# Optimization experiments

Hardware: AMD Instinct MI355X
Metric: run time of the kernel (lower is better)

## Reference

```python
import jax, jax.numpy as jnp
import numpy as np
from jax import lax

H = W = 1024            # input frame size
STRIDE = 16             # backbone total stride (4 stride-2 convs)
FH = FW = H // STRIDE   # 64x64 feature map
A = 3                   # anchors per cell
SIZES = (32.0, 64.0, 128.0)
K = 100                 # fixed NMS candidate count (jit-static)
SCORE_TH = 0.5          # kwargs['threshhold']
IOU_TH = 0.5
BORDER = 4              # draw_boxes border_size=4


def _conv(x, w, b, stride):
    y = lax.conv_general_dilated(x, w, (stride, stride), 'SAME',
                                 dimension_numbers=('NCHW', 'OIHW', 'NCHW'))
    return y + b[None, :, None, None]


def _anchors():
    ys, xs = jnp.meshgrid(jnp.arange(FH, dtype=jnp.float32),
                          jnp.arange(FW, dtype=jnp.float32), indexing='ij')
    cx = (xs + 0.5) * STRIDE
    cy = (ys + 0.5) * STRIDE
    sz = jnp.asarray(SIZES, dtype=jnp.float32)
    cx = jnp.broadcast_to(cx[:, :, None], (FH, FW, A))
    cy = jnp.broadcast_to(cy[:, :, None], (FH, FW, A))
    ww = jnp.broadcast_to(sz[None, None, :], (FH, FW, A))
    return jnp.stack([cx, cy, ww, ww], -1).reshape(-1, 4)  # [N,4] cx,cy,w,h


def _facenet(frame, w1, b1, w2, b2, w3, b3, w4, b4, wh, bh):
    x = jax.nn.relu(_conv(frame, w1, b1, 2))   # [1,32,512,512]
    x = jax.nn.relu(_conv(x, w2, b2, 2))       # [1,64,256,256]
    x = jax.nn.relu(_conv(x, w3, b3, 2))       # [1,128,128,128]
    x = jax.nn.relu(_conv(x, w4, b4, 2))       # [1,256,64,64]
    p = _conv(x, wh, bh, 1)                    # [1,A*5,64,64]
    p = p.reshape(A, 5, FH, FW).transpose(2, 3, 0, 1).reshape(-1, 5)  # [N,5]
    t, logit = p[:, :4], p[:, 4]
    a = _anchors()
    cx = a[:, 0] + t[:, 0] * a[:, 2]
    cy = a[:, 1] + t[:, 1] * a[:, 3]
    bw = a[:, 2] * jnp.exp(jnp.clip(t[:, 2], -4.0, 4.0))
    bhh = a[:, 3] * jnp.exp(jnp.clip(t[:, 3], -4.0, 4.0))
    boxes = jnp.stack([cx - bw * 0.5, cy - bhh * 0.5,
                       cx + bw * 0.5, cy + bhh * 0.5], -1)  # [N,4] xyxy
    scores = jax.nn.sigmoid(logit)             # [N]
    return boxes, scores


def _pairwise_iou(b):
    area = (b[:, 2] - b[:, 0]) * (b[:, 3] - b[:, 1])
    lt = jnp.maximum(b[:, None, :2], b[None, :, :2])
    rb = jnp.minimum(b[:, None, 2:], b[None, :, 2:])
    wh2 = jnp.clip(rb - lt, 0.0)
    inter = wh2[..., 0] * wh2[..., 1]
    return inter / (area[:, None] + area[None, :] - inter + 1e-9)


def _nms(boxes, scores):
    s = jnp.where(scores >= SCORE_TH, scores, -1.0)
    top, idx = lax.top_k(s, K)
    b = boxes[idx]                    # [K,4], score-sorted
    valid = top > 0.0
    ious = _pairwise_iou(b)           # [K,K]
    rng = jnp.arange(K)

    def body(i, keep):
        sup = (ious[i] > IOU_TH) & keep[i] & (rng > i)
        return keep & (~sup)

    keep = lax.fori_loop(0, K, body, valid)
    return b, keep


def _draw(frame, boxes, keep):
    x1 = jnp.clip(boxes[:, 0], 0.0, W)[:, None, None]
    y1 = jnp.clip(boxes[:, 1], 0.0, H)[:, None, None]
    x2 = jnp.clip(boxes[:, 2], 0.0, W)[:, None, None]
    y2 = jnp.clip(boxes[:, 3], 0.0, H)[:, None, None]
    ys = jnp.arange(H, dtype=jnp.float32)[None, :, None]
    xs = jnp.arange(W, dtype=jnp.float32)[None, None, :]
    inside = (ys >= y1) & (ys < y2) & (xs >= x1) & (xs < x2)
    inner = (ys >= y1 + BORDER) & (ys < y2 - BORDER) & \
            (xs >= x1 + BORDER) & (xs < x2 - BORDER)
    border = inside & (~inner) & keep[:, None, None]   # [K,H,W]
    mask = jnp.any(border, axis=0)                     # [H,W]
    red = jnp.array([1.0, 0.0, 0.0], dtype=frame.dtype)[None, :, None, None]
    return jnp.where(mask[None, None, :, :], red, frame)


def setup_inputs() -> dict:
    key = jax.random.key(0)
    ks = jax.random.split(key, 12)
    sc = 0.05
    return {
        'frame': jax.random.normal(ks[0], (1, 3, H, W), jnp.float32),
        'w1': jax.random.normal(ks[1], (32, 3, 3, 3), jnp.float32) * sc,
        'b1': jax.random.normal(ks[2], (32,), jnp.float32) * sc,
        'w2': jax.random.normal(ks[3], (64, 32, 3, 3), jnp.float32) * sc,
        'b2': jax.random.normal(ks[4], (64,), jnp.float32) * sc,
        'w3': jax.random.normal(ks[5], (128, 64, 3, 3), jnp.float32) * sc,
        'b3': jax.random.normal(ks[6], (128,), jnp.float32) * sc,
        'w4': jax.random.normal(ks[7], (256, 128, 3, 3), jnp.float32) * sc,
        'b4': jax.random.normal(ks[8], (256,), jnp.float32) * sc,
        'wh': jax.random.normal(ks[9], (A * 5, 256, 3, 3), jnp.float32) * sc,
        'bh': jax.random.normal(ks[10], (A * 5,), jnp.float32) * sc,
    }


def reference(frame, w1, b1, w2, b2, w3, b3, w4, b4, wh, bh):
    boxes, scores = _facenet(frame, w1, b1, w2, b2, w3, b3, w4, b4, wh, bh)
    kept_boxes, keep = _nms(boxes, scores)     # kwargs: use_nms=True, only_anchors=False
    im = _draw(frame, kept_boxes, keep)        # border_size=4, color='red'
    return im
```

## Files before the change

### kernel.cpp

```cpp
#include <hip/hip_runtime.h>


constexpr int KTOP  = 100;
constexpr int NANCH = 12288;

template<int CIN, int HIN, int WIN, int STRIDE, int COB, int CICHUNK, bool FUSEOUT>
__global__ __launch_bounds__(256)
void convk(const float* __restrict__ in, const float* __restrict__ w,
           const float* __restrict__ bias, float* __restrict__ out, int CO)
{
    constexpr int HOUT = (STRIDE == 2) ? HIN / 2 : HIN;
    constexpr int WOUT = (STRIDE == 2) ? WIN / 2 : WIN;
    constexpr int PADLO = (STRIDE == 1) ? 1 : 0;
    constexpr int NPX = HOUT * WOUT;

    const int px = blockIdx.x * 256 + threadIdx.x;
    const int oy = px / WOUT, ox = px % WOUT;
    const int co0 = blockIdx.y * COB;
    const int ci0 = blockIdx.z * CICHUNK;

    float acc[COB];
#pragma unroll
    for (int c = 0; c < COB; ++c) acc[c] = 0.f;

    const int iy0 = oy * STRIDE - PADLO, ix0 = ox * STRIDE - PADLO;
#pragma unroll 2
    for (int ci = ci0; ci < ci0 + CICHUNK; ++ci) {
        const float* __restrict__ ip = in + ci * (HIN * WIN);
        float v[9];
#pragma unroll
        for (int ky = 0; ky < 3; ++ky) {
            const int iy = iy0 + ky;
            const bool yok = (iy >= 0) && (iy < HIN);
#pragma unroll
            for (int kx = 0; kx < 3; ++kx) {
                const int ix = ix0 + kx;
                v[ky * 3 + kx] = (yok && ix >= 0 && ix < WIN) ? ip[iy * WIN + ix] : 0.f;
            }
        }
#pragma unroll
        for (int co = 0; co < COB; ++co) {
            const float* __restrict__ wp = w + ((co0 + co) * CIN + ci) * 9;
#pragma unroll
            for (int k = 0; k < 9; ++k)
                acc[co] = fmaf(v[k], wp[k], acc[co]);
        }
    }
    if constexpr (FUSEOUT) {
#pragma unroll
        for (int co = 0; co < COB; ++co)
            out[(co0 + co) * NPX + px] = fmaxf(acc[co] + bias[co0 + co], 0.f);
    } else {
#pragma unroll
        for (int co = 0; co < COB; ++co)
            out[(blockIdx.z * CO + co0 + co) * NPX + px] = acc[co];
    }
}

template<int NCHUNK, int NPX, bool RELU>
__global__ __launch_bounds__(256)
void reducek(const float* __restrict__ part, const float* __restrict__ bias,
             float* __restrict__ out, int CO)
{
    const int t = blockIdx.x * 256 + threadIdx.x;
    const int co = t / NPX, px = t - co * NPX;
    float s = 0.f;
#pragma unroll
    for (int c = 0; c < NCHUNK; ++c) s += part[(c * CO + co) * NPX + px];
    s += bias[co];
    out[co * NPX + px] = RELU ? fmaxf(s, 0.f) : s;
}

__global__ void decode_kernel(const float* __restrict__ head,
                              float4* __restrict__ boxes,
                              unsigned long long* __restrict__ keys)
{
    const int i = blockIdx.x * 256 + threadIdx.x;
    const int a = i % 3;
    const int xy = i / 3;
    const int x = xy & 63, y = xy >> 6;
    const int px = y * 64 + x;

    const float t0 = head[(a * 5 + 0) * 4096 + px];
    const float t1 = head[(a * 5 + 1) * 4096 + px];
    const float t2 = head[(a * 5 + 2) * 4096 + px];
    const float t3 = head[(a * 5 + 3) * 4096 + px];
    const float lg = head[(a * 5 + 4) * 4096 + px];

    const float sz  = (a == 0) ? 32.f : (a == 1) ? 64.f : 128.f;
    const float cxa = (x + 0.5f) * 16.f;
    const float cya = (y + 0.5f) * 16.f;

    const float cx = __fadd_rn(cxa, __fmul_rn(t0, sz));
    const float cy = __fadd_rn(cya, __fmul_rn(t1, sz));
    const float bw = __fmul_rn(sz, expf(fminf(fmaxf(t2, -4.f), 4.f)));
    const float bh = __fmul_rn(sz, expf(fminf(fmaxf(t3, -4.f), 4.f)));
    const float hw = __fmul_rn(bw, 0.5f);
    const float hh = __fmul_rn(bh, 0.5f);

    float4 bb;
    bb.x = __fsub_rn(cx, hw);
    bb.y = __fsub_rn(cy, hh);
    bb.z = __fadd_rn(cx, hw);
    bb.w = __fadd_rn(cy, hh);
    boxes[i] = bb;

    const float score = 1.f / (1.f + expf(-lg));
    unsigned long long key = 0ull;
    if (score >= 0.5f) {
        key = ((unsigned long long)__float_as_uint(score) << 32)
            | (unsigned long long)(0xFFFFFFFFu - (unsigned)i);
    }
    keys[i] = key;
}

constexpr int JSPLIT = 16;
constexpr int JCHUNK = NANCH / JSPLIT;

__global__ __launch_bounds__(256)
void rank_kernel(const unsigned long long* __restrict__ keys,
                 int* __restrict__ rank)
{
    const int i = blockIdx.x * 256 + threadIdx.x;
    const unsigned long long ki = keys[i];
    const int lane = threadIdx.x & 63;
    const int jbase = blockIdx.y * JCHUNK;

    int cnt = 0;
    for (int g = 0; g < JCHUNK / 64; ++g) {
        const unsigned long long kj = keys[jbase + g * 64 + lane];
        const unsigned lo0 = (unsigned)kj;
        const unsigned hi0 = (unsigned)(kj >> 32);
#pragma unroll
        for (int l = 0; l < 64; ++l) {
            const unsigned lo = (unsigned)__builtin_amdgcn_readlane((int)lo0, l);
            const unsigned hi = (unsigned)__builtin_amdgcn_readlane((int)hi0, l);
            const unsigned long long kjj = ((unsigned long long)hi << 32) | lo;
            cnt += (kjj > ki) ? 1 : 0;
        }
    }
    if (cnt) atomicAdd(&rank[i], cnt);
}

__global__ void scatter_kernel(const unsigned long long* __restrict__ keys,
                               const int* __restrict__ rank,
                               const float4* __restrict__ boxes,
                               float4* __restrict__ selb, int* __restrict__ selv)
{
    const int i = blockIdx.x * 256 + threadIdx.x;
    if (keys[i] == 0ull) return;
    const int r = rank[i];
    if (r < KTOP) { selb[r] = boxes[i]; selv[r] = 1; }
}

__global__ __launch_bounds__(128)
void nms_kernel(const float4* __restrict__ selb, const int* __restrict__ selv,
                float4* __restrict__ drawb)
{
    __shared__ float bx1[KTOP], by1[KTOP], bx2[KTOP], by2[KTOP], ar[KTOP];
    __shared__ int kp[KTOP];
    const int t = threadIdx.x;
    if (t < KTOP) {
        const float4 b = selb[t];
        bx1[t] = b.x; by1[t] = b.y; bx2[t] = b.z; by2[t] = b.w;
        ar[t] = (b.z - b.x) * (b.w - b.y);
        kp[t] = selv[t];
    }
    __syncthreads();
    for (int i = 0; i < KTOP - 1; ++i) {
        if (t > i && t < KTOP) {
            if (kp[i] && kp[t]) {
                const float lx = fmaxf(bx1[i], bx1[t]);
                const float ly = fmaxf(by1[i], by1[t]);
                const float rx = fminf(bx2[i], bx2[t]);
                const float ry = fminf(by2[i], by2[t]);
                const float ww = fmaxf(rx - lx, 0.f);
                const float hh = fmaxf(ry - ly, 0.f);
                const float inter = ww * hh;
                const float iou = inter / (ar[i] + ar[t] - inter + 1e-9f);
                if (iou > 0.5f) kp[t] = 0;
            }
        }
        __syncthreads();
    }
    if (t < KTOP) {
        float4 d;
        if (kp[t]) {
            d.x = fminf(fmaxf(bx1[t], 0.f), 1024.f);
            d.y = fminf(fmaxf(by1[t], 0.f), 1024.f);
            d.z = fminf(fmaxf(bx2[t], 0.f), 1024.f);
            d.w = fminf(fmaxf(by2[t], 0.f), 1024.f);
        } else {
            d.x = 3e9f; d.y = 3e9f; d.z = -3e9f; d.w = -3e9f;
        }
        drawb[t] = d;
    }
}

__global__ __launch_bounds__(256)
void draw_kernel(const float* __restrict__ frame,
                 const float4* __restrict__ drawb, float* __restrict__ out)
{
    const int y = blockIdx.x >> 2;
    const int x = ((blockIdx.x & 3) << 8) + threadIdx.x;
    const float fy = (float)y, fx = (float)x;

    bool mask = false;
#pragma unroll 1
    for (int b = 0; b < KTOP; ++b) {
        const float4 d = drawb[b];
        if (fy >= d.y && fy < d.w) {
            const bool yinner = (fy >= d.y + 4.f) && (fy < d.w - 4.f);
            const bool xin    = (fx >= d.x) && (fx < d.z);
            const bool xinner = (fx >= d.x + 4.f) && (fx < d.z - 4.f);
            mask |= xin && !(yinner && xinner);
        }
    }
    const int p = y * 1024 + x;
    const float f0 = frame[p];
    const float f1 = frame[1048576 + p];
    const float f2 = frame[2097152 + p];
    out[p]           = mask ? 1.f : f0;
    out[1048576 + p] = mask ? 0.f : f1;
    out[2097152 + p] = mask ? 0.f : f2;
}

extern "C" void kernel_launch(void* const* d_in, const int* in_sizes, int n_in,
                              void* d_out, int out_size, void* d_ws, size_t ws_size,
                              hipStream_t stream)
{
    const float* frame = (const float*)d_in[0];
    const float* w1 = (const float*)d_in[1];  const float* b1 = (const float*)d_in[2];
    const float* w2 = (const float*)d_in[3];  const float* b2 = (const float*)d_in[4];
    const float* w3 = (const float*)d_in[5];  const float* b3 = (const float*)d_in[6];
    const float* w4 = (const float*)d_in[7];  const float* b4 = (const float*)d_in[8];
    const float* wh = (const float*)d_in[9];  const float* bh = (const float*)d_in[10];

    char* ws = (char*)d_ws;
    float* buf1  = (float*)ws;
    float* buf2  = (float*)(ws + 33554432);
    float* part3 = (float*)ws;
    float* buf3  = (float*)(ws + 16777216);
    float* part4 = (float*)(ws + 33554432);
    float* buf4  = (float*)ws;
    float* partH = (float*)(ws + 8388608);
    float* heado = (float*)(ws + 16777216);
    char*  B     = ws + 33554432;
    float4* boxes = (float4*)(B);
    unsigned long long* keys = (unsigned long long*)(B + 196608);
    int*    rankb = (int*)(B + 294912);
    int*    selv  = (int*)(B + 344064);
    float4* selb  = (float4*)(B + 344576);
    float4* drawb = (float4*)(B + 346176);
    float*  outp  = (float*)d_out;

    convk<3, 1024, 1024, 2, 8, 3,  true ><<<dim3(1024, 4, 1), 256, 0, stream>>>(frame, w1, b1, buf1, 32);
    convk<32, 512,  512, 2, 8, 32, true ><<<dim3(256,  8, 1), 256, 0, stream>>>(buf1, w2, b2, buf2, 64);
    convk<64, 256,  256, 2, 8, 32, false><<<dim3(64,  16, 2), 256, 0, stream>>>(buf2, w3, nullptr, part3, 128);
    reducek<2, 16384, true><<<8192, 256, 0, stream>>>(part3, b3, buf3, 128);
    convk<128, 128, 128, 2, 8, 32, false><<<dim3(16,  32, 4), 256, 0, stream>>>(buf3, w4, nullptr, part4, 256);
    reducek<4, 4096, true><<<4096, 256, 0, stream>>>(part4, b4, buf4, 256);

    convk<256, 64, 64, 1, 5, 16, false><<<dim3(16, 3, 16), 256, 0, stream>>>(buf4, wh, nullptr, partH, 15);
    reducek<16, 4096, false><<<240, 256, 0, stream>>>(partH, bh, heado, 15);

    hipMemsetAsync(rankb, 0, 49152 + 512, stream);

    decode_kernel<<<48, 256, 0, stream>>>(heado, boxes, keys);
    rank_kernel<<<dim3(48, JSPLIT), 256, 0, stream>>>(keys, rankb);
    scatter_kernel<<<48, 256, 0, stream>>>(keys, rankb, boxes, selb, selv);
    nms_kernel<<<1, 128, 0, stream>>>(selb, selv, drawb);
    draw_kernel<<<4096, 256, 0, stream>>>(frame, drawb, outp);
}
```

Measured before the change: 450.8 us.

## Register-tile convolutions over multiple output pixels with vectorized row loads

The direct convolution kernel now computes PXT adjacent output pixels per thread. It loads each input row segment once, with float4 loads for the stride-2 layers, and reuses those values across pixels and output channels. Outputs are written as float4 stores. Per-layer grid shapes and channel blocking are retuned, the head conv uses all 15 output channels per block with a 64-way input-channel split, and workspace offsets are reshuffled to fit. Register pressure rises with the COB×PXT accumulators, and the head's partial-sum buffer grows, which adds reduce traffic.

Result: faster. 423.7 us (-6.0%).

```diff
diff --git a/kernel.cpp b/kernel.cpp
--- a/kernel.cpp
+++ b/kernel.cpp
@@ -4,56 +4,86 @@
 constexpr int KTOP  = 100;
 constexpr int NANCH = 12288;
 
-template<int CIN, int HIN, int WIN, int STRIDE, int COB, int CICHUNK, bool FUSEOUT>
+template<int CIN, int HIN, int WIN, int STRIDE, int PXT, int COB, int CICHUNK, bool FUSEOUT>
 __global__ __launch_bounds__(256)
 void convk(const float* __restrict__ in, const float* __restrict__ w,
            const float* __restrict__ bias, float* __restrict__ out, int CO)
 {
     constexpr int HOUT = (STRIDE == 2) ? HIN / 2 : HIN;
     constexpr int WOUT = (STRIDE == 2) ? WIN / 2 : WIN;
-    constexpr int PADLO = (STRIDE == 1) ? 1 : 0;
-    constexpr int NPX = HOUT * WOUT;
-
-    const int px = blockIdx.x * 256 + threadIdx.x;
-    const int oy = px / WOUT, ox = px % WOUT;
+    constexpr int NPX  = HOUT * WOUT;
+    constexpr int GPR  = WOUT / PXT;
+    constexpr int NCOL = (STRIDE == 2) ? 2 * PXT + 1 : PXT + 2;
+
+    const int g   = blockIdx.x * 256 + threadIdx.x;
+    const int oy  = g / GPR;
+    const int oxb = (g - oy * GPR) * PXT;
     const int co0 = blockIdx.y * COB;
     const int ci0 = blockIdx.z * CICHUNK;
 
-    float acc[COB];
-#pragma unroll
-    for (int c = 0; c < COB; ++c) acc[c] = 0.f;
-
-    const int iy0 = oy * STRIDE - PADLO, ix0 = ox * STRIDE - PADLO;
-#pragma unroll 2
+    float acc[COB][PXT];
+#pragma unroll
+    for (int c = 0; c < COB; ++c)
+#pragma unroll
+        for (int p = 0; p < PXT; ++p) acc[c][p] = 0.f;
+
+    const int iy0 = oy * STRIDE - ((STRIDE == 1) ? 1 : 0);
+    const int ixb = oxb * STRIDE - ((STRIDE == 1) ? 1 : 0);
+
     for (int ci = ci0; ci < ci0 + CICHUNK; ++ci) {
-        const float* __restrict__ ip = in + ci * (HIN * WIN);
-        float v[9];
 #pragma unroll
         for (int ky = 0; ky < 3; ++ky) {
             const int iy = iy0 + ky;
-            const bool yok = (iy >= 0) && (iy < HIN);
-#pragma unroll
-            for (int kx = 0; kx < 3; ++kx) {
-                const int ix = ix0 + kx;
-                v[ky * 3 + kx] = (yok && ix >= 0 && ix < WIN) ? ip[iy * WIN + ix] : 0.f;
+            const float* __restrict__ rp = in + ((size_t)ci * HIN + iy) * WIN;
+            float c[NCOL];
+            if (iy >= 0 && iy < HIN) {
+                if constexpr (STRIDE == 2) {
+                    const float4 q0 = *reinterpret_cast<const float4*>(rp + ixb);
+                    const float4 q1 = *reinterpret_cast<const float4*>(rp + ixb + 4);
+                    c[0] = q0.x; c[1] = q0.y; c[2] = q0.z; c[3] = q0.w;
+                    c[4] = q1.x; c[5] = q1.y; c[6] = q1.z; c[7] = q1.w;
+                    c[8] = (ixb + 8 < WIN) ? rp[ixb + 8] : 0.f;
+                } else {
+                    c[0] = (ixb >= 0) ? rp[ixb] : 0.f;
+                    c[1] = rp[ixb + 1];
+                    c[2] = (ixb + 2 < WIN) ? rp[ixb + 2] : 0.f;
+                }
+            } else {
+#pragma unroll
+                for (int k = 0; k < NCOL; ++k) c[k] = 0.f;
             }
-        }
-#pragma unroll
-        for (int co = 0; co < COB; ++co) {
-            const float* __restrict__ wp = w + ((co0 + co) * CIN + ci) * 9;
-#pragma unroll
-            for (int k = 0; k < 9; ++k)
-                acc[co] = fmaf(v[k], wp[k], acc[co]);
-        }
-    }
-    if constexpr (FUSEOUT) {
-#pragma unroll
-        for (int co = 0; co < COB; ++co)
-            out[(co0 + co) * NPX + px] = fmaxf(acc[co] + bias[co0 + co], 0.f);
-    } else {
-#pragma unroll
-        for (int co = 0; co < COB; ++co)
-            out[(blockIdx.z * CO + co0 + co) * NPX + px] = acc[co];
+#pragma unroll
+            for (int co = 0; co < COB; ++co) {
+                const float* __restrict__ wp = w + (((size_t)(co0 + co) * CIN + ci) * 3 + ky) * 3;
+#pragma unroll
+                for (int kx = 0; kx < 3; ++kx) {
+                    const float wv = wp[kx];
+#pragma unroll
+                    for (int p = 0; p < PXT; ++p)
+                        acc[co][p] = fmaf(c[STRIDE * p + kx], wv, acc[co][p]);
+                }
+            }
+        }
+    }
+
+    const int obase = oy * WOUT + oxb;
+#pragma unroll
+    for (int co = 0; co < COB; ++co) {
+        float r[PXT];
+#pragma unroll
+        for (int p = 0; p < PXT; ++p) {
+            r[p] = FUSEOUT ? fmaxf(acc[co][p] + bias[co0 + co], 0.f) : acc[co][p];
+        }
+        float* __restrict__ op = FUSEOUT
+            ? out + (size_t)(co0 + co) * NPX + obase
+            : out + ((size_t)blockIdx.z * CO + co0 + co) * NPX + obase;
+        if constexpr (PXT == 4) {
+            float4 q; q.x = r[0]; q.y = r[1]; q.z = r[2]; q.w = r[3];
+            *reinterpret_cast<float4*>(op) = q;
+        } else {
+#pragma unroll
+            for (int p = 0; p < PXT; ++p) op[p] = r[p];
+        }
     }
 }
 
@@ -66,9 +96,9 @@
     const int co = t / NPX, px = t - co * NPX;
     float s = 0.f;
 #pragma unroll
-    for (int c = 0; c < NCHUNK; ++c) s += part[(c * CO + co) * NPX + px];
+    for (int c = 0; c < NCHUNK; ++c) s += part[((size_t)c * CO + co) * NPX + px];
     s += bias[co];
-    out[co * NPX + px] = RELU ? fmaxf(s, 0.f) : s;
+    out[(size_t)co * NPX + px] = RELU ? fmaxf(s, 0.f) : s;
 }
 
 __global__ void decode_kernel(const float* __restrict__ head,
@@ -241,10 +271,10 @@
     float* buf2  = (float*)(ws + 33554432);
     float* part3 = (float*)ws;
     float* buf3  = (float*)(ws + 16777216);
-    float* part4 = (float*)(ws + 33554432);
-    float* buf4  = (float*)ws;
-    float* partH = (float*)(ws + 8388608);
-    float* heado = (float*)(ws + 16777216);
+    float* part4 = (float*)ws;
+    float* buf4  = (float*)(ws + 25165824);
+    float* partH = (float*)ws;
+    float* heado = (float*)(ws + 29360128);
     char*  B     = ws + 33554432;
     float4* boxes = (float4*)(B);
     unsigned long long* keys = (unsigned long long*)(B + 196608);
@@ -254,15 +284,15 @@
     float4* drawb = (float4*)(B + 346176);
     float*  outp  = (float*)d_out;
 
-    convk<3, 1024, 1024, 2, 8, 3,  true ><<<dim3(1024, 4, 1), 256, 0, stream>>>(frame, w1, b1, buf1, 32);
-    convk<32, 512,  512, 2, 8, 32, true ><<<dim3(256,  8, 1), 256, 0, stream>>>(buf1, w2, b2, buf2, 64);
-    convk<64, 256,  256, 2, 8, 32, false><<<dim3(64,  16, 2), 256, 0, stream>>>(buf2, w3, nullptr, part3, 128);
+    convk<3, 1024, 1024, 2, 4, 8, 3,  true ><<<dim3(256,  4, 1), 256, 0, stream>>>(frame, w1, b1, buf1, 32);
+    convk<32,  512,  512, 2, 4, 4, 32, true ><<<dim3(64,  16, 1), 256, 0, stream>>>(buf1, w2, b2, buf2, 64);
+    convk<64,  256,  256, 2, 4, 4, 32, false><<<dim3(16,  32, 2), 256, 0, stream>>>(buf2, w3, nullptr, part3, 128);
     reducek<2, 16384, true><<<8192, 256, 0, stream>>>(part3, b3, buf3, 128);
-    convk<128, 128, 128, 2, 8, 32, false><<<dim3(16,  32, 4), 256, 0, stream>>>(buf3, w4, nullptr, part4, 256);
+    convk<128, 128,  128, 2, 4, 4, 32, false><<<dim3(4,   64, 4), 256, 0, stream>>>(buf3, w4, nullptr, part4, 256);
     reducek<4, 4096, true><<<4096, 256, 0, stream>>>(part4, b4, buf4, 256);
 
-    convk<256, 64, 64, 1, 5, 16, false><<<dim3(16, 3, 16), 256, 0, stream>>>(buf4, wh, nullptr, partH, 15);
-    reducek<16, 4096, false><<<240, 256, 0, stream>>>(partH, bh, heado, 15);
+    convk<256, 64, 64, 1, 1, 15, 4, false><<<dim3(16, 1, 64), 256, 0, stream>>>(buf4, wh, nullptr, partH, 15);
+    reducek<64, 4096, false><<<240, 256, 0, stream>>>(partH, bh, heado, 15);
 
     hipMemsetAsync(rankb, 0, 49152 + 512, stream);
 
```

## Restructure conv inner loop with row-segment indexing, float2 loads, and retuned head split

Applied to the files above, without the earlier changes.

The conv kernel now maps each 64-lane wavefront to a contiguous output row segment and precomputes clamped row offsets and masks. For stride-2 layers it loads an adjacent pair with one float2 read plus one scalar read per kernel row, and it interleaves the FMAs per row. The inner loop is no longer unrolled by 2. The head conv now computes all 15 output channels per block and splits input channels 32 ways, and workspace offsets are reshuffled to fit the larger partial buffer. This aims to cut address arithmetic and boundary checks and to reuse each input load across more output channels, but it adds a larger reduction in the head stage.

Measured after the change: 403.7 us. 10.5% less time.

```diff
diff --git a/kernel.cpp b/kernel.cpp
--- a/kernel.cpp
+++ b/kernel.cpp
@@ -11,49 +11,85 @@
 {
     constexpr int HOUT = (STRIDE == 2) ? HIN / 2 : HIN;
     constexpr int WOUT = (STRIDE == 2) ? WIN / 2 : WIN;
-    constexpr int PADLO = (STRIDE == 1) ? 1 : 0;
-    constexpr int NPX = HOUT * WOUT;
-
-    const int px = blockIdx.x * 256 + threadIdx.x;
-    const int oy = px / WOUT, ox = px % WOUT;
-    const int co0 = blockIdx.y * COB;
-    const int ci0 = blockIdx.z * CICHUNK;
+    constexpr int NPX  = HOUT * WOUT;
+    constexpr int SPR  = WOUT / 64;
+
+    const int lane = threadIdx.x & 63;
+    const int seg  = blockIdx.x * 4 + (threadIdx.x >> 6);
+    const int oy   = seg / SPR;
+    const int ox   = (seg - oy * SPR) * 64 + lane;
+    const int co0  = blockIdx.y * COB;
+    const int ci0  = blockIdx.z * CICHUNK;
 
     float acc[COB];
 #pragma unroll
     for (int c = 0; c < COB; ++c) acc[c] = 0.f;
 
-    const int iy0 = oy * STRIDE - PADLO, ix0 = ox * STRIDE - PADLO;
-#pragma unroll 2
-    for (int ci = ci0; ci < ci0 + CICHUNK; ++ci) {
-        const float* __restrict__ ip = in + ci * (HIN * WIN);
-        float v[9];
+    size_t ro[3];
+    bool   rm[3];
+#pragma unroll
+    for (int ky = 0; ky < 3; ++ky) {
+        const int iy = (STRIDE == 2) ? (2 * oy + ky) : (oy + ky - 1);
+        rm[ky] = (iy >= 0) && (iy < HIN);
+        const int iyc = iy < 0 ? 0 : (iy > HIN - 1 ? HIN - 1 : iy);
+        ro[ky] = (size_t)iyc * WIN;
+    }
+    int  xa, xb, xc;
+    bool ma, mc;
+    if constexpr (STRIDE == 2) {
+        xa = 2 * ox;
+        xb = 0;
+        mc = (2 * ox + 2) < WIN;
+        xc = mc ? 2 * ox + 2 : WIN - 1;
+        ma = true;
+    } else {
+        ma = ox > 0;
+        xa = ma ? ox - 1 : 0;
+        xb = ox;
+        mc = ox < WIN - 1;
+        xc = mc ? ox + 1 : WIN - 1;
+    }
+
+    for (int cii = 0; cii < CICHUNK; ++cii) {
+        const int ci = ci0 + cii;
+        const float* __restrict__ cp = in + (size_t)ci * (HIN * WIN);
 #pragma unroll
         for (int ky = 0; ky < 3; ++ky) {
-            const int iy = iy0 + ky;
-            const bool yok = (iy >= 0) && (iy < HIN);
-#pragma unroll
-            for (int kx = 0; kx < 3; ++kx) {
-                const int ix = ix0 + kx;
-                v[ky * 3 + kx] = (yok && ix >= 0 && ix < WIN) ? ip[iy * WIN + ix] : 0.f;
+            float t0, t1, t2;
+            if constexpr (STRIDE == 2) {
+                const float2 p = *reinterpret_cast<const float2*>(cp + ro[ky] + xa);
+                const float  e = cp[ro[ky] + xc];
+                t0 = rm[ky] ? p.x : 0.f;
+                t1 = rm[ky] ? p.y : 0.f;
+                t2 = (rm[ky] && mc) ? e : 0.f;
+            } else {
+                const float a = cp[ro[ky] + xa];
+                const float b = cp[ro[ky] + xb];
+                const float e = cp[ro[ky] + xc];
+                t0 = (rm[ky] && ma) ? a : 0.f;
+                t1 = rm[ky] ? b : 0.f;
+                t2 = (rm[ky] && mc) ? e : 0.f;
             }
-        }
-#pragma unroll
-        for (int co = 0; co < COB; ++co) {
-            const float* __restrict__ wp = w + ((co0 + co) * CIN + ci) * 9;
-#pragma unroll
-            for (int k = 0; k < 9; ++k)
-                acc[co] = fmaf(v[k], wp[k], acc[co]);
-        }
-    }
-    if constexpr (FUSEOUT) {
-#pragma unroll
-        for (int co = 0; co < COB; ++co)
-            out[(co0 + co) * NPX + px] = fmaxf(acc[co] + bias[co0 + co], 0.f);
-    } else {
-#pragma unroll
-        for (int co = 0; co < COB; ++co)
-            out[(blockIdx.z * CO + co0 + co) * NPX + px] = acc[co];
+#pragma unroll
+            for (int co = 0; co < COB; ++co) {
+                const float* __restrict__ wp =
+                    w + (((size_t)(co0 + co) * CIN + ci) * 3 + ky) * 3;
+                acc[co] = fmaf(t0, wp[0], acc[co]);
+                acc[co] = fmaf(t1, wp[1], acc[co]);
+                acc[co] = fmaf(t2, wp[2], acc[co]);
+            }
+        }
+    }
+
+    const int op = oy * WOUT + ox;
+#pragma unroll
+    for (int co = 0; co < COB; ++co) {
+        if constexpr (FUSEOUT) {
+            out[(size_t)(co0 + co) * NPX + op] =
+                fmaxf(acc[co] + bias[co0 + co], 0.f);
+        } else {
+            out[((size_t)blockIdx.z * CO + co0 + co) * NPX + op] = acc[co];
+        }
     }
 }
 
@@ -66,9 +102,9 @@
     const int co = t / NPX, px = t - co * NPX;
     float s = 0.f;
 #pragma unroll
-    for (int c = 0; c < NCHUNK; ++c) s += part[(c * CO + co) * NPX + px];
+    for (int c = 0; c < NCHUNK; ++c) s += part[((size_t)c * CO + co) * NPX + px];
     s += bias[co];
-    out[co * NPX + px] = RELU ? fmaxf(s, 0.f) : s;
+    out[(size_t)co * NPX + px] = RELU ? fmaxf(s, 0.f) : s;
 }
 
 __global__ void decode_kernel(const float* __restrict__ head,
@@ -241,28 +277,30 @@
     float* buf2  = (float*)(ws + 33554432);
     float* part3 = (float*)ws;
     float* buf3  = (float*)(ws + 16777216);
-    float* part4 = (float*)(ws + 33554432);
-    float* buf4  = (float*)ws;
-    float* partH = (float*)(ws + 8388608);
-    float* heado = (float*)(ws + 16777216);
-    char*  B     = ws + 33554432;
-    float4* boxes = (float4*)(B);
-    unsigned long long* keys = (unsigned long long*)(B + 196608);
-    int*    rankb = (int*)(B + 294912);
-    int*    selv  = (int*)(B + 344064);
-    float4* selb  = (float4*)(B + 344576);
-    float4* drawb = (float4*)(B + 346176);
+    float* part4 = (float*)ws;
+    float* buf4  = (float*)(ws + 25165824);
+    float* partH = (float*)ws;
+    float* heado = (float*)(ws + 8388608);
+    char*  D     = ws + 33554432;
+    float4* boxes = (float4*)(D);
+    unsigned long long* keys = (unsigned long long*)(D + 196608);
+    int*    rankb = (int*)(D + 294912);
+    int*    selv  = (int*)(D + 344064);
+    float4* selb  = (float4*)(D + 344576);
+    float4* drawb = (float4*)(D + 346176);
     float*  outp  = (float*)d_out;
 
-    convk<3, 1024, 1024, 2, 8, 3,  true ><<<dim3(1024, 4, 1), 256, 0, stream>>>(frame, w1, b1, buf1, 32);
-    convk<32, 512,  512, 2, 8, 32, true ><<<dim3(256,  8, 1), 256, 0, stream>>>(buf1, w2, b2, buf2, 64);
-    convk<64, 256,  256, 2, 8, 32, false><<<dim3(64,  16, 2), 256, 0, stream>>>(buf2, w3, nullptr, part3, 128);
+    convk<3,  1024, 1024, 2, 8, 3,  true ><<<dim3(1024, 4, 1), 256, 0, stream>>>(frame, w1, b1, buf1, 32);
+    convk<32,  512,  512, 2, 8, 32, true ><<<dim3(256,  8, 1), 256, 0, stream>>>(buf1, w2, b2, buf2, 64);
+
+    convk<64,  256,  256, 2, 8, 32, false><<<dim3(64, 16, 2), 256, 0, stream>>>(buf2, w3, nullptr, part3, 128);
     reducek<2, 16384, true><<<8192, 256, 0, stream>>>(part3, b3, buf3, 128);
-    convk<128, 128, 128, 2, 8, 32, false><<<dim3(16,  32, 4), 256, 0, stream>>>(buf3, w4, nullptr, part4, 256);
+
+    convk<128, 128,  128, 2, 8, 32, false><<<dim3(16, 32, 4), 256, 0, stream>>>(buf3, w4, nullptr, part4, 256);
     reducek<4, 4096, true><<<4096, 256, 0, stream>>>(part4, b4, buf4, 256);
 
-    convk<256, 64, 64, 1, 5, 16, false><<<dim3(16, 3, 16), 256, 0, stream>>>(buf4, wh, nullptr, partH, 15);
-    reducek<16, 4096, false><<<240, 256, 0, stream>>>(partH, bh, heado, 15);
+    convk<256, 64, 64, 1, 15, 8, false><<<dim3(16, 1, 32), 256, 0, stream>>>(buf4, wh, nullptr, partH, 15);
+    reducek<32, 4096, false><<<240, 256, 0, stream>>>(partH, bh, heado, 15);
 
     hipMemsetAsync(rankb, 0, 49152 + 512, stream);
 
```
